# Optimization experiments

Hardware: AMD Instinct MI355X
Metric: run time of the kernel (lower is better)

The kernel has to match this reference:

```python
import jax, jax.numpy as jnp
import numpy as np
from jax import lax

H = 32  # hidden size


def _lstm_layer(x, Wih, Whh, bih, bhh):
    """x: [B, T, D_in]; returns [B, T, H]. PyTorch gate order i,f,g,o."""
    B = x.shape[0]
    b = bih + bhh  # [4H]
    # precompute input projections for all timesteps: [T, B, 4H]
    xp = jnp.einsum('btd,gd->tbg', x, Wih) + b

    def step(carry, xt):
        h, c = carry
        gates = xt + h @ Whh.T  # [B, 4H]
        i, f, g, o = jnp.split(gates, 4, axis=-1)
        i = jax.nn.sigmoid(i)
        f = jax.nn.sigmoid(f)
        g = jnp.tanh(g)
        o = jax.nn.sigmoid(o)
        c = f * c + i * g
        h = o * jnp.tanh(c)
        return (h, c), h

    init = (jnp.zeros((B, H), x.dtype), jnp.zeros((B, H), x.dtype))
    _, ys = lax.scan(step, init, xp)  # ys: [T, B, H]
    return jnp.swapaxes(ys, 0, 1)


def _lstm5(x, Wih0, Wih_rest, Whh, bih, bhh):
    h = _lstm_layer(x, Wih0, Whh[0], bih[0], bhh[0])
    for l in range(4):  # fixed small layer count
        h = _lstm_layer(h, Wih_rest[l], Whh[l + 1], bih[l + 1], bhh[l + 1])
    return h


def setup_inputs() -> dict:
    key = jax.random.key(0)
    ks = jax.random.split(key, 18)
    s = 1.0 / np.sqrt(H)
    B, T = 16384, 20
    u = lambda k, shp: jax.random.uniform(k, shp, jnp.float32, -s, s)
    return {
        'accel': jax.random.normal(ks[0], (B, T, 3), jnp.float32),
        'gyro': jax.random.normal(ks[1], (B, T, 3), jnp.float32),
        'accel_Wih0': u(ks[2], (4 * H, 3)),
        'accel_Wih_rest': u(ks[3], (4, 4 * H, H)),
        'accel_Whh': u(ks[4], (5, 4 * H, H)),
        'accel_bih': u(ks[5], (5, 4 * H)),
        'accel_bhh': u(ks[6], (5, 4 * H)),
        'gyro_Wih0': u(ks[7], (4 * H, 3)),
        'gyro_Wih_rest': u(ks[8], (4, 4 * H, H)),
        'gyro_Whh': u(ks[9], (5, 4 * H, H)),
        'gyro_bih': u(ks[10], (5, 4 * H)),
        'gyro_bhh': u(ks[11], (5, 4 * H)),
        'fc1_w': u(ks[12], (128, T * H * 2)),
        'fc1_b': u(ks[13], (128,)),
        'fc2_w': u(ks[14], (5, 128)),
        'fc2_b': u(ks[15], (5,)),
    }


def reference(accel, gyro, accel_Wih0, accel_Wih_rest, accel_Whh, accel_bih,
              accel_bhh, gyro_Wih0, gyro_Wih_rest, gyro_Whh, gyro_bih,
              gyro_bhh, fc1_w, fc1_b, fc2_w, fc2_b):
    a = _lstm5(accel, accel_Wih0, accel_Wih_rest, accel_Whh, accel_bih, accel_bhh)
    g = _lstm5(gyro, gyro_Wih0, gyro_Wih_rest, gyro_Whh, gyro_bih, gyro_bhh)
    x = jnp.concatenate([a, g], axis=1)          # [B, 2T, H]
    x = x.reshape(x.shape[0], -1)                # [B, 2*T*H]
    x = jax.nn.relu(x @ fc1_w.T + fc1_b)         # [B, 128]
    return x @ fc2_w.T + fc2_b                   # [B, 5]
```

## Files before the change

### kernel.cpp

```cpp
#include <hip/hip_runtime.h>
#include <math.h>

#define B_TOTAL 16384
#define T_STEPS 20
#define NGRP    1024

typedef __attribute__((ext_vector_type(8))) __bf16 bf16x8;
typedef __attribute__((ext_vector_type(4))) float f32x4;

__device__ __forceinline__ float sigf(float x) {
    return __builtin_amdgcn_rcpf(1.0f + __expf(-x));
}
__device__ __forceinline__ float tanhf_fast(float x) {
    return fmaf(-2.0f, __builtin_amdgcn_rcpf(__expf(2.0f * x) + 1.0f), 1.0f);
}

__device__ __forceinline__ __bf16 bf16_bits(unsigned short s) {
    __bf16 r; __builtin_memcpy(&r, &s, 2); return r;
}
__device__ __forceinline__ void split_trunc(float x, __bf16& hi, __bf16& lo) {
    unsigned u = __float_as_uint(x);
    hi = bf16_bits((unsigned short)(u >> 16));
    float l = x - __uint_as_float(u & 0xFFFF0000u);
    lo = bf16_bits((unsigned short)(__float_as_uint(l) >> 16));
}

__global__ __launch_bounds__(256, 4)
void lstm5_mfma(const float* __restrict__ accel, const float* __restrict__ gyro,
                const float* __restrict__ aWih0, const float* __restrict__ aWihR,
                const float* __restrict__ aWhh,  const float* __restrict__ aBih,
                const float* __restrict__ aBhh,
                const float* __restrict__ gWih0, const float* __restrict__ gWihR,
                const float* __restrict__ gWhh,  const float* __restrict__ gBih,
                const float* __restrict__ gBhh,
                __bf16* __restrict__ Xhi, __bf16* __restrict__ Xlo) {
    const int tid  = threadIdx.x;
    const int w    = tid >> 6;
    const int lane = tid & 63;
    const int e    = lane & 15;
    const int quad = lane >> 4;
    const int sensor = blockIdx.y;
    const int bbase  = blockIdx.x * 16;

    const float* xin  = sensor ? gyro  : accel;
    const float* Wih0 = sensor ? gWih0 : aWih0;
    const float* WihR = sensor ? gWihR : aWihR;
    const float* Whh  = sensor ? gWhh  : aWhh;
    const float* Bih  = sensor ? gBih  : aBih;
    const float* Bhh  = sensor ? gBhh  : aBhh;

    __shared__ __align__(16) __bf16 shi[20 * 512];
    __shared__ __align__(16) __bf16 slo[20 * 512];

    const int ug0 = w * 8 + quad;
    const int ug1 = w * 8 + 4 + quad;

    const int m_row   = lane & 15;
    const int orow_t0 = (m_row & 3) * 32 + (w * 8 + (m_row >> 2));
    const int orow_t1 = (m_row & 3) * 32 + (w * 8 + 4 + (m_row >> 2));

    bf16x8 wih_h0, wih_l0, wih_h1, wih_l1;
    bf16x8 whh_h0, whh_l0, whh_h1, whh_l1;
    f32x4  bias0v, bias1v;
    float  c0 = 0.f, c1 = 0.f;

#define LOAD_FRAG(Wsrc, orow, fh, fl)                         \
    {                                                         \
        const float* p_ = (Wsrc) + (orow) * 32 + quad * 8;    \
        _Pragma("unroll")                                     \
        for (int jj = 0; jj < 8; ++jj) {                      \
            __bf16 h_, l_;                                    \
            split_trunc(p_[jj], h_, l_);                      \
            (fh)[jj] = h_;  (fl)[jj] = l_;                    \
        }                                                     \
    }

#define LOAD_BIAS(l)                                                        \
    {                                                                       \
        _Pragma("unroll")                                                   \
        for (int r = 0; r < 4; ++r) {                                       \
            bias0v[r] = Bih[(l) * 128 + r * 32 + ug0] + Bhh[(l) * 128 + r * 32 + ug0]; \
            bias1v[r] = Bih[(l) * 128 + r * 32 + ug1] + Bhh[(l) * 128 + r * 32 + ug1]; \
        }                                                                   \
    }

#define ACT_STORE(t)                                                        \
    {                                                                       \
        float i0 = sigf(acc0[0]), f0 = sigf(acc0[1]);                       \
        float g0 = tanhf_fast(acc0[2]), o0 = sigf(acc0[3]);                 \
        c0 = f0 * c0 + i0 * g0;                                             \
        float h0 = o0 * tanhf_fast(c0);                                     \
        float i1 = sigf(acc1[0]), f1 = sigf(acc1[1]);                       \
        float g1 = tanhf_fast(acc1[2]), o1 = sigf(acc1[3]);                 \
        c1 = f1 * c1 + i1 * g1;                                             \
        float h1 = o1 * tanhf_fast(c1);                                     \
        __syncthreads();             \
        int i0x = (t) * 512 + w * 128 + e * 8 + quad;                       \
        int i1x = i0x + 4;                                                  \
        __bf16 hh_, ll_;                                                    \
        split_trunc(h0, hh_, ll_);  shi[i0x] = hh_;  slo[i0x] = ll_;        \
        split_trunc(h1, hh_, ll_);  shi[i1x] = hh_;  slo[i1x] = ll_;        \
        __syncthreads();       \
    }

    {
        LOAD_FRAG(Whh, orow_t0, whh_h0, whh_l0);
        LOAD_FRAG(Whh, orow_t1, whh_h1, whh_l1);
        LOAD_BIAS(0);
        float w0reg[2][4][3];
#pragma unroll
        for (int r = 0; r < 4; ++r)
#pragma unroll
            for (int k = 0; k < 3; ++k) {
                w0reg[0][r][k] = Wih0[(r * 32 + ug0) * 3 + k];
                w0reg[1][r][k] = Wih0[(r * 32 + ug1) * 3 + k];
            }
        const float* xrow = xin + (size_t)(bbase + e) * (T_STEPS * 3);

        for (int t = 0; t < T_STEPS; ++t) {
            float x0 = xrow[t * 3 + 0];
            float x1 = xrow[t * 3 + 1];
            float x2 = xrow[t * 3 + 2];
            f32x4 acc0 = bias0v;
            f32x4 acc1 = bias1v;
#pragma unroll
            for (int r = 0; r < 4; ++r) {
                acc0[r] = fmaf(w0reg[0][r][0], x0,
                          fmaf(w0reg[0][r][1], x1,
                          fmaf(w0reg[0][r][2], x2, acc0[r])));
                acc1[r] = fmaf(w0reg[1][r][0], x0,
                          fmaf(w0reg[1][r][1], x1,
                          fmaf(w0reg[1][r][2], x2, acc1[r])));
            }
            if (t > 0) {
                int rb = (t - 1) * 512 + quad * 128 + e * 8;
                bf16x8 bh = *(const bf16x8*)&shi[rb];
                bf16x8 bl = *(const bf16x8*)&slo[rb];
                acc0 = __builtin_amdgcn_mfma_f32_16x16x32_bf16(whh_h0, bh, acc0, 0, 0, 0);
                acc0 = __builtin_amdgcn_mfma_f32_16x16x32_bf16(whh_h0, bl, acc0, 0, 0, 0);
                acc0 = __builtin_amdgcn_mfma_f32_16x16x32_bf16(whh_l0, bh, acc0, 0, 0, 0);
                acc1 = __builtin_amdgcn_mfma_f32_16x16x32_bf16(whh_h1, bh, acc1, 0, 0, 0);
                acc1 = __builtin_amdgcn_mfma_f32_16x16x32_bf16(whh_h1, bl, acc1, 0, 0, 0);
                acc1 = __builtin_amdgcn_mfma_f32_16x16x32_bf16(whh_l1, bh, acc1, 0, 0, 0);
            }
            ACT_STORE(t);
        }
    }

    for (int l = 1; l < 5; ++l) {
        const float* Wi = WihR + (l - 1) * 4096;
        const float* Wh = Whh + l * 4096;
        LOAD_FRAG(Wi, orow_t0, wih_h0, wih_l0);
        LOAD_FRAG(Wi, orow_t1, wih_h1, wih_l1);
        LOAD_FRAG(Wh, orow_t0, whh_h0, whh_l0);
        LOAD_FRAG(Wh, orow_t1, whh_h1, whh_l1);
        LOAD_BIAS(l);
        c0 = 0.f; c1 = 0.f;

        for (int t = 0; t < T_STEPS; ++t) {
            f32x4 acc0, acc1;
            {
                int rb = t * 512 + quad * 128 + e * 8;
                bf16x8 bh = *(const bf16x8*)&shi[rb];
                bf16x8 bl = *(const bf16x8*)&slo[rb];
                acc0 = __builtin_amdgcn_mfma_f32_16x16x32_bf16(wih_h0, bh, bias0v, 0, 0, 0);
                acc0 = __builtin_amdgcn_mfma_f32_16x16x32_bf16(wih_h0, bl, acc0, 0, 0, 0);
                acc0 = __builtin_amdgcn_mfma_f32_16x16x32_bf16(wih_l0, bh, acc0, 0, 0, 0);
                acc1 = __builtin_amdgcn_mfma_f32_16x16x32_bf16(wih_h1, bh, bias1v, 0, 0, 0);
                acc1 = __builtin_amdgcn_mfma_f32_16x16x32_bf16(wih_h1, bl, acc1, 0, 0, 0);
                acc1 = __builtin_amdgcn_mfma_f32_16x16x32_bf16(wih_l1, bh, acc1, 0, 0, 0);
            }
            if (t > 0) {
                int rb = (t - 1) * 512 + quad * 128 + e * 8;
                bf16x8 bh = *(const bf16x8*)&shi[rb];
                bf16x8 bl = *(const bf16x8*)&slo[rb];
                acc0 = __builtin_amdgcn_mfma_f32_16x16x32_bf16(whh_h0, bh, acc0, 0, 0, 0);
                acc0 = __builtin_amdgcn_mfma_f32_16x16x32_bf16(whh_h0, bl, acc0, 0, 0, 0);
                acc0 = __builtin_amdgcn_mfma_f32_16x16x32_bf16(whh_l0, bh, acc0, 0, 0, 0);
                acc1 = __builtin_amdgcn_mfma_f32_16x16x32_bf16(whh_h1, bh, acc1, 0, 0, 0);
                acc1 = __builtin_amdgcn_mfma_f32_16x16x32_bf16(whh_h1, bl, acc1, 0, 0, 0);
                acc1 = __builtin_amdgcn_mfma_f32_16x16x32_bf16(whh_l1, bh, acc1, 0, 0, 0);
            }
            ACT_STORE(t);
        }
    }
    __syncthreads();

    {
        size_t base = ((size_t)(sensor * NGRP + blockIdx.x)) * (20 * 512);
        float4* dh = (float4*)(Xhi + base);
        float4* dl = (float4*)(Xlo + base);
        const float4* sh = (const float4*)shi;
        const float4* sl = (const float4*)slo;
        for (int i = tid; i < 20 * 512 / 8; i += 256) { dh[i] = sh[i]; dl[i] = sl[i]; }
    }
#undef LOAD_FRAG
#undef LOAD_BIAS
#undef ACT_STORE
}

__global__ void w1_prep(const float* __restrict__ w1,
                        __bf16* __restrict__ w1ah, __bf16* __restrict__ w1al) {
    int t = blockIdx.x * blockDim.x + threadIdx.x;
    if (t >= 20480) return;
    int lane = t & 63;
    int ks   = (t >> 6) % 40;
    int mt   = t / (64 * 40);
    int row  = mt * 16 + (lane & 15);
    int col0 = ks * 32 + (lane >> 4) * 8;
    const float* src = w1 + row * 1280 + col0;
#pragma unroll
    for (int j = 0; j < 8; ++j) {
        __bf16 h_, l_;
        split_trunc(src[j], h_, l_);
        w1ah[t * 8 + j] = h_;
        w1al[t * 8 + j] = l_;
    }
}

__global__ __launch_bounds__(512, 2)
void fc_mfma(const __bf16* __restrict__ Xhi, const __bf16* __restrict__ Xlo,
             const __bf16* __restrict__ w1ah, const __bf16* __restrict__ w1al,
             const float* __restrict__ fc1_b, const float* __restrict__ fc2_w,
             const float* __restrict__ fc2_b, float* __restrict__ out) {
    const int tid   = threadIdx.x;
    const int wv    = tid >> 6;
    const int lane  = tid & 63;
    const int e     = lane & 15;
    const int quad  = lane >> 4;
    const int cg    = wv & 3;
    const int mhalf = wv >> 2;

    __shared__ float sred[2][64][5];

    const int g = blockIdx.x * 4 + cg;

    f32x4 acc[4];
#pragma unroll
    for (int m = 0; m < 4; ++m) acc[m] = (f32x4){0.f, 0.f, 0.f, 0.f};

    for (int sensor = 0; sensor < 2; ++sensor) {
        const __bf16* bh_base = Xhi + ((size_t)(sensor * NGRP + g)) * (20 * 512) + lane * 8;
        const __bf16* bl_base = Xlo + ((size_t)(sensor * NGRP + g)) * (20 * 512) + lane * 8;
        for (int t = 0; t < T_STEPS; ++t) {
            int ks = sensor * 20 + t;
            bf16x8 bh = *(const bf16x8*)(bh_base + t * 512);
            bf16x8 bl = *(const bf16x8*)(bl_base + t * 512);
#pragma unroll
            for (int m = 0; m < 4; ++m) {
                int mt = mhalf * 4 + m;
                const __bf16* ap = w1ah + ((size_t)(mt * 40 + ks) * 64 + lane) * 8;
                const __bf16* al = w1al + ((size_t)(mt * 40 + ks) * 64 + lane) * 8;
                bf16x8 ah = *(const bf16x8*)ap;
                bf16x8 av = *(const bf16x8*)al;
                acc[m] = __builtin_amdgcn_mfma_f32_16x16x32_bf16(ah, bh, acc[m], 0, 0, 0);
                acc[m] = __builtin_amdgcn_mfma_f32_16x16x32_bf16(ah, bl, acc[m], 0, 0, 0);
                acc[m] = __builtin_amdgcn_mfma_f32_16x16x32_bf16(av, bh, acc[m], 0, 0, 0);
            }
        }
    }

    float p[5] = {0.f, 0.f, 0.f, 0.f, 0.f};
#pragma unroll
    for (int m = 0; m < 4; ++m) {
        int mt = mhalf * 4 + m;
#pragma unroll
        for (int r = 0; r < 4; ++r) {
            int row = mt * 16 + quad * 4 + r;
            float v = fmaxf(acc[m][r] + fc1_b[row], 0.f);
#pragma unroll
            for (int n = 0; n < 5; ++n) p[n] = fmaf(v, fc2_w[n * 128 + row], p[n]);
        }
    }
#pragma unroll
    for (int n = 0; n < 5; ++n) {
        p[n] += __shfl_xor(p[n], 16, 64);
        p[n] += __shfl_xor(p[n], 32, 64);
    }
    if (quad == 0) {
#pragma unroll
        for (int n = 0; n < 5; ++n) sred[mhalf][cg * 16 + e][n] = p[n];
    }
    __syncthreads();
    if (tid < 320) {
        int col = tid / 5, n = tid - col * 5;
        out[(size_t)(blockIdx.x * 64 + col) * 5 + n] =
            sred[0][col][n] + sred[1][col][n] + fc2_b[n];
    }
}

extern "C" void kernel_launch(void* const* d_in, const int* in_sizes, int n_in,
                              void* d_out, int out_size, void* d_ws, size_t ws_size,
                              hipStream_t stream) {
    const float* accel  = (const float*)d_in[0];
    const float* gyro   = (const float*)d_in[1];
    const float* aWih0  = (const float*)d_in[2];
    const float* aWihR  = (const float*)d_in[3];
    const float* aWhh   = (const float*)d_in[4];
    const float* aBih   = (const float*)d_in[5];
    const float* aBhh   = (const float*)d_in[6];
    const float* gWih0  = (const float*)d_in[7];
    const float* gWihR  = (const float*)d_in[8];
    const float* gWhh   = (const float*)d_in[9];
    const float* gBih   = (const float*)d_in[10];
    const float* gBhh   = (const float*)d_in[11];
    const float* fc1_w  = (const float*)d_in[12];
    const float* fc1_b  = (const float*)d_in[13];
    const float* fc2_w  = (const float*)d_in[14];
    const float* fc2_b  = (const float*)d_in[15];
    float* out = (float*)d_out;

    const size_t XN = (size_t)2 * NGRP * 20 * 512;
    __bf16* Xhi  = (__bf16*)d_ws;
    __bf16* Xlo  = Xhi + XN;
    __bf16* W1ah = Xlo + XN;
    __bf16* W1al = W1ah + 163840;

    hipLaunchKernelGGL(w1_prep, dim3(80), dim3(256), 0, stream, fc1_w, W1ah, W1al);

    hipLaunchKernelGGL(lstm5_mfma, dim3(NGRP, 2), dim3(256), 0, stream,
                       accel, gyro, aWih0, aWihR, aWhh, aBih, aBhh,
                       gWih0, gWihR, gWhh, gBih, gBhh, Xhi, Xlo);

    hipLaunchKernelGGL(fc_mfma, dim3(B_TOTAL / 64), dim3(512), 0, stream,
                       Xhi, Xlo, W1ah, W1al, fc1_b, fc2_w, fc2_b, out);
}
```

Before: 317.3 us.

## Split FC1 reduction over K across waves with LDS accumulation

Restructures the fc_mfma kernel so each 256-thread block handles one group of 16 batch columns, with its four waves each taking a quarter of the K dimension and all 8 output-row tiles. Partial accumulators are combined through shared memory before the bias, ReLU and fc2 epilogue. The grid grows from 256 to 1024 blocks, which is meant to give more parallelism and better occupancy on the small FC stage. The cost is more accumulator registers per wave, an extra LDS reduction pass with a barrier, and each wave loading all eight W1 row tiles per k-step.

```diff
diff --git a/kernel.cpp b/kernel.cpp
--- a/kernel.cpp
+++ b/kernel.cpp
@@ -218,56 +218,61 @@
     }
 }
 
-__global__ __launch_bounds__(512, 2)
+__global__ __launch_bounds__(256, 4)
 void fc_mfma(const __bf16* __restrict__ Xhi, const __bf16* __restrict__ Xlo,
              const __bf16* __restrict__ w1ah, const __bf16* __restrict__ w1al,
              const float* __restrict__ fc1_b, const float* __restrict__ fc2_w,
              const float* __restrict__ fc2_b, float* __restrict__ out) {
-    const int tid   = threadIdx.x;
-    const int wv    = tid >> 6;
-    const int lane  = tid & 63;
-    const int e     = lane & 15;
-    const int quad  = lane >> 4;
-    const int cg    = wv & 3;
-    const int mhalf = wv >> 2;
-
-    __shared__ float sred[2][64][5];
-
-    const int g = blockIdx.x * 4 + cg;
-
-    f32x4 acc[4];
-#pragma unroll
-    for (int m = 0; m < 4; ++m) acc[m] = (f32x4){0.f, 0.f, 0.f, 0.f};
-
-    for (int sensor = 0; sensor < 2; ++sensor) {
-        const __bf16* bh_base = Xhi + ((size_t)(sensor * NGRP + g)) * (20 * 512) + lane * 8;
-        const __bf16* bl_base = Xlo + ((size_t)(sensor * NGRP + g)) * (20 * 512) + lane * 8;
-        for (int t = 0; t < T_STEPS; ++t) {
-            int ks = sensor * 20 + t;
-            bf16x8 bh = *(const bf16x8*)(bh_base + t * 512);
-            bf16x8 bl = *(const bf16x8*)(bl_base + t * 512);
-#pragma unroll
-            for (int m = 0; m < 4; ++m) {
-                int mt = mhalf * 4 + m;
-                const __bf16* ap = w1ah + ((size_t)(mt * 40 + ks) * 64 + lane) * 8;
-                const __bf16* al = w1al + ((size_t)(mt * 40 + ks) * 64 + lane) * 8;
-                bf16x8 ah = *(const bf16x8*)ap;
-                bf16x8 av = *(const bf16x8*)al;
-                acc[m] = __builtin_amdgcn_mfma_f32_16x16x32_bf16(ah, bh, acc[m], 0, 0, 0);
-                acc[m] = __builtin_amdgcn_mfma_f32_16x16x32_bf16(ah, bl, acc[m], 0, 0, 0);
-                acc[m] = __builtin_amdgcn_mfma_f32_16x16x32_bf16(av, bh, acc[m], 0, 0, 0);
-            }
-        }
-    }
+    const int tid  = threadIdx.x;
+    const int wv   = tid >> 6;
+    const int lane = tid & 63;
+    const int e    = lane & 15;
+    const int quad = lane >> 4;
+    const int g    = blockIdx.x;
+
+    __shared__ __align__(16) f32x4 sacc[4][8][64];
+    __shared__ float sred[4][16][5];
+
+    f32x4 acc[8];
+#pragma unroll
+    for (int m = 0; m < 8; ++m) acc[m] = (f32x4){0.f, 0.f, 0.f, 0.f};
+
+    for (int kk = 0; kk < 10; ++kk) {
+        int ks = wv * 10 + kk;
+        int sensor = ks / 20, t = ks % 20;
+        size_t bb = ((size_t)(sensor * NGRP + g)) * (20 * 512) + t * 512 + lane * 8;
+        bf16x8 bh = *(const bf16x8*)(Xhi + bb);
+        bf16x8 bl = *(const bf16x8*)(Xlo + bb);
+#pragma unroll
+        for (int m = 0; m < 8; ++m) {
+            const __bf16* ap = w1ah + ((size_t)((m * 40 + ks) * 64 + lane)) * 8;
+            const __bf16* al = w1al + ((size_t)((m * 40 + ks) * 64 + lane)) * 8;
+            bf16x8 ah = *(const bf16x8*)ap;
+            bf16x8 av = *(const bf16x8*)al;
+            acc[m] = __builtin_amdgcn_mfma_f32_16x16x32_bf16(ah, bh, acc[m], 0, 0, 0);
+            acc[m] = __builtin_amdgcn_mfma_f32_16x16x32_bf16(ah, bl, acc[m], 0, 0, 0);
+            acc[m] = __builtin_amdgcn_mfma_f32_16x16x32_bf16(av, bh, acc[m], 0, 0, 0);
+        }
+    }
+#pragma unroll
+    for (int m = 0; m < 8; ++m) sacc[wv][m][lane] = acc[m];
+    __syncthreads();
 
     float p[5] = {0.f, 0.f, 0.f, 0.f, 0.f};
 #pragma unroll
-    for (int m = 0; m < 4; ++m) {
-        int mt = mhalf * 4 + m;
+    for (int mm = 0; mm < 2; ++mm) {
+        int mt = wv * 2 + mm;
+        f32x4 z = sacc[0][mt][lane];
+#pragma unroll
+        for (int k = 1; k < 4; ++k) {
+            f32x4 zz = sacc[k][mt][lane];
+#pragma unroll
+            for (int r = 0; r < 4; ++r) z[r] += zz[r];
+        }
 #pragma unroll
         for (int r = 0; r < 4; ++r) {
             int row = mt * 16 + quad * 4 + r;
-            float v = fmaxf(acc[m][r] + fc1_b[row], 0.f);
+            float v = fmaxf(z[r] + fc1_b[row], 0.f);
 #pragma unroll
             for (int n = 0; n < 5; ++n) p[n] = fmaf(v, fc2_w[n * 128 + row], p[n]);
         }
@@ -279,13 +284,13 @@
     }
     if (quad == 0) {
 #pragma unroll
-        for (int n = 0; n < 5; ++n) sred[mhalf][cg * 16 + e][n] = p[n];
+        for (int n = 0; n < 5; ++n) sred[wv][e][n] = p[n];
     }
     __syncthreads();
-    if (tid < 320) {
+    if (tid < 80) {
         int col = tid / 5, n = tid - col * 5;
-        out[(size_t)(blockIdx.x * 64 + col) * 5 + n] =
-            sred[0][col][n] + sred[1][col][n] + fc2_b[n];
+        out[(size_t)(g * 16 + col) * 5 + n] =
+            sred[0][col][n] + sred[1][col][n] + sred[2][col][n] + sred[3][col][n] + fc2_b[n];
     }
 }
 
@@ -322,6 +327,6 @@
                        accel, gyro, aWih0, aWihR, aWhh, aBih, aBhh,
                        gWih0, gWihR, gWhh, gBih, gBhh, Xhi, Xlo);
 
-    hipLaunchKernelGGL(fc_mfma, dim3(B_TOTAL / 64), dim3(512), 0, stream,
+    hipLaunchKernelGGL(fc_mfma, dim3(NGRP), dim3(256), 0, stream,
                        Xhi, Xlo, W1ah, W1al, fc1_b, fc2_w, fc2_b, out);
 }
```

Result: faster. 291.7 us (-8.1%).

## Fuse fc1 partial GEMM into LSTM kernel epilogue, add small finish kernel

Applied to the files above, without the earlier changes.

Each LSTM block now multiplies its final-layer hidden states, still in shared memory, by its sensor's half of fc1 using split-bf16 MFMA. It writes fp32 partial fc1 pre-activations instead of the full hi/lo bf16 hidden sequences. A lightweight finish kernel sums the two sensor partials, applies bias and ReLU, and computes fc2. This removes the large intermediate activation round-trip through global memory, at the cost of extra global weight loads and MFMA work in the LSTM kernel's tail.

```diff
diff --git a/kernel.cpp b/kernel.cpp
--- a/kernel.cpp
+++ b/kernel.cpp
@@ -33,7 +33,8 @@
                 const float* __restrict__ gWih0, const float* __restrict__ gWihR,
                 const float* __restrict__ gWhh,  const float* __restrict__ gBih,
                 const float* __restrict__ gBhh,
-                __bf16* __restrict__ Xhi, __bf16* __restrict__ Xlo) {
+                const __bf16* __restrict__ w1ah, const __bf16* __restrict__ w1al,
+                float* __restrict__ Zpart ) {
     const int tid  = threadIdx.x;
     const int w    = tid >> 6;
     const int lane = tid & 63;
@@ -187,12 +188,33 @@
     __syncthreads();
 
     {
-        size_t base = ((size_t)(sensor * NGRP + blockIdx.x)) * (20 * 512);
-        float4* dh = (float4*)(Xhi + base);
-        float4* dl = (float4*)(Xlo + base);
-        const float4* sh = (const float4*)shi;
-        const float4* sl = (const float4*)slo;
-        for (int i = tid; i < 20 * 512 / 8; i += 256) { dh[i] = sh[i]; dl[i] = sl[i]; }
+        f32x4 zacc0 = (f32x4){0.f, 0.f, 0.f, 0.f};
+        f32x4 zacc1 = (f32x4){0.f, 0.f, 0.f, 0.f};
+        const int mt0 = w * 2, mt1 = w * 2 + 1;
+        for (int t = 0; t < T_STEPS; ++t) {
+            int rb = t * 512 + quad * 128 + e * 8;
+            bf16x8 bh = *(const bf16x8*)&shi[rb];
+            bf16x8 bl = *(const bf16x8*)&slo[rb];
+            int ks = sensor * 20 + t;
+            size_t ab0 = ((size_t)((mt0 * 40 + ks) * 64 + lane)) * 8;
+            size_t ab1 = ((size_t)((mt1 * 40 + ks) * 64 + lane)) * 8;
+            bf16x8 ah0 = *(const bf16x8*)(w1ah + ab0);
+            bf16x8 al0 = *(const bf16x8*)(w1al + ab0);
+            bf16x8 ah1 = *(const bf16x8*)(w1ah + ab1);
+            bf16x8 al1 = *(const bf16x8*)(w1al + ab1);
+            zacc0 = __builtin_amdgcn_mfma_f32_16x16x32_bf16(ah0, bh, zacc0, 0, 0, 0);
+            zacc0 = __builtin_amdgcn_mfma_f32_16x16x32_bf16(ah0, bl, zacc0, 0, 0, 0);
+            zacc0 = __builtin_amdgcn_mfma_f32_16x16x32_bf16(al0, bh, zacc0, 0, 0, 0);
+            zacc1 = __builtin_amdgcn_mfma_f32_16x16x32_bf16(ah1, bh, zacc1, 0, 0, 0);
+            zacc1 = __builtin_amdgcn_mfma_f32_16x16x32_bf16(ah1, bl, zacc1, 0, 0, 0);
+            zacc1 = __builtin_amdgcn_mfma_f32_16x16x32_bf16(al1, bh, zacc1, 0, 0, 0);
+        }
+        float* zp = Zpart + ((size_t)(sensor * NGRP + blockIdx.x)) * 2048;
+#pragma unroll
+        for (int r = 0; r < 4; ++r) {
+            zp[mt0 * 256 + (quad * 4 + r) * 16 + e] = zacc0[r];
+            zp[mt1 * 256 + (quad * 4 + r) * 16 + e] = zacc1[r];
+        }
     }
 #undef LOAD_FRAG
 #undef LOAD_BIAS
@@ -218,74 +240,36 @@
     }
 }
 
-__global__ __launch_bounds__(512, 2)
-void fc_mfma(const __bf16* __restrict__ Xhi, const __bf16* __restrict__ Xlo,
-             const __bf16* __restrict__ w1ah, const __bf16* __restrict__ w1al,
-             const float* __restrict__ fc1_b, const float* __restrict__ fc2_w,
-             const float* __restrict__ fc2_b, float* __restrict__ out) {
-    const int tid   = threadIdx.x;
-    const int wv    = tid >> 6;
-    const int lane  = tid & 63;
-    const int e     = lane & 15;
-    const int quad  = lane >> 4;
-    const int cg    = wv & 3;
-    const int mhalf = wv >> 2;
-
-    __shared__ float sred[2][64][5];
-
-    const int g = blockIdx.x * 4 + cg;
-
-    f32x4 acc[4];
-#pragma unroll
-    for (int m = 0; m < 4; ++m) acc[m] = (f32x4){0.f, 0.f, 0.f, 0.f};
-
-    for (int sensor = 0; sensor < 2; ++sensor) {
-        const __bf16* bh_base = Xhi + ((size_t)(sensor * NGRP + g)) * (20 * 512) + lane * 8;
-        const __bf16* bl_base = Xlo + ((size_t)(sensor * NGRP + g)) * (20 * 512) + lane * 8;
-        for (int t = 0; t < T_STEPS; ++t) {
-            int ks = sensor * 20 + t;
-            bf16x8 bh = *(const bf16x8*)(bh_base + t * 512);
-            bf16x8 bl = *(const bf16x8*)(bl_base + t * 512);
-#pragma unroll
-            for (int m = 0; m < 4; ++m) {
-                int mt = mhalf * 4 + m;
-                const __bf16* ap = w1ah + ((size_t)(mt * 40 + ks) * 64 + lane) * 8;
-                const __bf16* al = w1al + ((size_t)(mt * 40 + ks) * 64 + lane) * 8;
-                bf16x8 ah = *(const bf16x8*)ap;
-                bf16x8 av = *(const bf16x8*)al;
-                acc[m] = __builtin_amdgcn_mfma_f32_16x16x32_bf16(ah, bh, acc[m], 0, 0, 0);
-                acc[m] = __builtin_amdgcn_mfma_f32_16x16x32_bf16(ah, bl, acc[m], 0, 0, 0);
-                acc[m] = __builtin_amdgcn_mfma_f32_16x16x32_bf16(av, bh, acc[m], 0, 0, 0);
-            }
-        }
-    }
-
+__global__ __launch_bounds__(256, 8)
+void fc_finish(const float* __restrict__ Zpart, const float* __restrict__ fc1_b,
+               const float* __restrict__ fc2_w, const float* __restrict__ fc2_b,
+               float* __restrict__ out) {
+    const int tid = threadIdx.x;
+    const int e   = tid & 15;
+    const int rt  = tid >> 4;
+    const int g   = blockIdx.x;
+    __shared__ float sp[16][16][5];
+
+    const float* z0 = Zpart + (size_t)g * 2048;
+    const float* z1 = Zpart + (size_t)(NGRP + g) * 2048;
     float p[5] = {0.f, 0.f, 0.f, 0.f, 0.f};
 #pragma unroll
-    for (int m = 0; m < 4; ++m) {
-        int mt = mhalf * 4 + m;
-#pragma unroll
-        for (int r = 0; r < 4; ++r) {
-            int row = mt * 16 + quad * 4 + r;
-            float v = fmaxf(acc[m][r] + fc1_b[row], 0.f);
-#pragma unroll
-            for (int n = 0; n < 5; ++n) p[n] = fmaf(v, fc2_w[n * 128 + row], p[n]);
-        }
-    }
-#pragma unroll
-    for (int n = 0; n < 5; ++n) {
-        p[n] += __shfl_xor(p[n], 16, 64);
-        p[n] += __shfl_xor(p[n], 32, 64);
-    }
-    if (quad == 0) {
-#pragma unroll
-        for (int n = 0; n < 5; ++n) sred[mhalf][cg * 16 + e][n] = p[n];
-    }
+    for (int rr = 0; rr < 8; ++rr) {
+        int row = rt * 8 + rr;
+        int zi  = (row >> 4) * 256 + (row & 15) * 16 + e;
+        float v = fmaxf(z0[zi] + z1[zi] + fc1_b[row], 0.f);
+#pragma unroll
+        for (int n = 0; n < 5; ++n) p[n] = fmaf(v, fc2_w[n * 128 + row], p[n]);
+    }
+#pragma unroll
+    for (int n = 0; n < 5; ++n) sp[rt][e][n] = p[n];
     __syncthreads();
-    if (tid < 320) {
+    if (tid < 80) {
         int col = tid / 5, n = tid - col * 5;
-        out[(size_t)(blockIdx.x * 64 + col) * 5 + n] =
-            sred[0][col][n] + sred[1][col][n] + fc2_b[n];
+        float s = fc2_b[n];
+#pragma unroll
+        for (int k = 0; k < 16; ++k) s += sp[k][col][n];
+        out[(size_t)(g * 16 + col) * 5 + n] = s;
     }
 }
 
@@ -310,18 +294,16 @@
     const float* fc2_b  = (const float*)d_in[15];
     float* out = (float*)d_out;
 
-    const size_t XN = (size_t)2 * NGRP * 20 * 512;
-    __bf16* Xhi  = (__bf16*)d_ws;
-    __bf16* Xlo  = Xhi + XN;
-    __bf16* W1ah = Xlo + XN;
+    __bf16* W1ah = (__bf16*)d_ws;
     __bf16* W1al = W1ah + 163840;
+    float*  Zpart = (float*)(W1al + 163840);
 
     hipLaunchKernelGGL(w1_prep, dim3(80), dim3(256), 0, stream, fc1_w, W1ah, W1al);
 
     hipLaunchKernelGGL(lstm5_mfma, dim3(NGRP, 2), dim3(256), 0, stream,
                        accel, gyro, aWih0, aWihR, aWhh, aBih, aBhh,
-                       gWih0, gWihR, gWhh, gBih, gBhh, Xhi, Xlo);
-
-    hipLaunchKernelGGL(fc_mfma, dim3(B_TOTAL / 64), dim3(512), 0, stream,
-                       Xhi, Xlo, W1ah, W1al, fc1_b, fc2_w, fc2_b, out);
-}
+                       gWih0, gWihR, gWhh, gBih, gBhh, W1ah, W1al, Zpart);
+
+    hipLaunchKernelGGL(fc_finish, dim3(NGRP), dim3(256), 0, stream,
+                       Zpart, fc1_b, fc2_w, fc2_b, out);
+}
```

Measured after the change: 292.6 us. -7.8%, faster.
